# Optimization experiments

Hardware: AMD Instinct MI355X
Metric: run time of the kernel (lower is better)

The kernel has to match this reference:

```python
import jax, jax.numpy as jnp
from jax import lax
import numpy as np

NODE = 5
LAST_F = 64  # hidden_size // node_num = 320 // 5
EPS = 1e-5


def setup_inputs() -> dict:
    key = jax.random.key(0)
    ks = jax.random.split(key, 16)
    B, T = 8192, 512
    x = jax.random.normal(ks[0], (B, NODE, 1, T), dtype=jnp.float32)
    adj = jax.random.bernoulli(ks[1], 0.5, (NODE, NODE)).astype(jnp.float32)
    g = 0.02  # xavier gain in reset_parameters
    W0 = jax.random.normal(ks[2], (65, 128), jnp.float32) * g
    b0 = jnp.zeros((128,), jnp.float32)
    W1 = jax.random.normal(ks[3], (128, 128), jnp.float32) * g
    b1 = jnp.zeros((128,), jnp.float32)
    W2 = jax.random.normal(ks[4], (128, LAST_F), jnp.float32) * g
    b2 = jnp.zeros((LAST_F,), jnp.float32)
    fc1_w = jax.random.normal(ks[5], (NODE + NODE * LAST_F, 256), jnp.float32) * 0.05
    fc1_b = jnp.zeros((256,), jnp.float32)
    bn_gamma = jnp.ones((256,), jnp.float32)
    bn_beta = jnp.zeros((256,), jnp.float32)
    fc2_w = jax.random.normal(ks[6], (256, 7), jnp.float32) * 0.05
    fc2_b = jnp.zeros((7,), jnp.float32)
    return dict(x=x, adj=adj, W0=W0, b0=b0, W1=W1, b1=b1, W2=W2, b2=b2,
                fc1_w=fc1_w, fc1_b=fc1_b, bn_gamma=bn_gamma, bn_beta=bn_beta,
                fc2_w=fc2_w, fc2_b=fc2_b)


def reference(x, adj, W0, b0, W1, b1, W2, b2, fc1_w, fc1_b, bn_gamma, bn_beta, fc2_w, fc2_b):
    B = x.shape[0]
    T = x.shape[3]
    # [B, node, 1, T] -> [T, B, node]
    xt = jnp.transpose(x.reshape(B, NODE, T), (2, 0, 1))
    A = adj.T  # module stores adj.t()

    def gcn(h, W, b):
        # support = h @ W ; out = A @ support + b   (batched)
        return jnp.einsum('ij,bjf->bif', A, h @ W) + b

    def step(state, x_t):
        h = jnp.concatenate([x_t[:, :, None], state], axis=2)  # [B, node, 1+LAST_F]
        h = jax.nn.relu(gcn(h, W0, b0))
        h = jax.nn.relu(gcn(h, W1, b1))
        h = jnp.tanh(gcn(h, W2, b2))
        return h, None

    state0 = jnp.zeros((B, NODE, LAST_F), x.dtype)
    state, _ = lax.scan(step, state0, xt)

    x_end = xt[-1]  # [B, node]
    xs = jnp.concatenate([x_end, state.reshape(B, -1)], axis=1)  # [B, node+hidden]
    h = jax.nn.relu(xs @ fc1_w + fc1_b)
    # BatchNorm1d in training mode: batch statistics (biased variance)
    mean = jnp.mean(h, axis=0)
    var = jnp.var(h, axis=0)
    h = (h - mean) * jax.lax.rsqrt(var + EPS) * bn_gamma + bn_beta
    logits = h @ fc2_w + fc2_b
    return jax.nn.softmax(logits, axis=1)
```

## Files before the change

kernel.cpp:

```cpp
#include <hip/hip_runtime.h>
#include <math.h>

#define NODE 5
#define TT 512
#define NBATCH 8192
#define NB 16
#define MR (NB*NODE)
#define TB 32
#define XS_DIM 325
#define H2 256
#define EPS 1e-5f

typedef _Float16 h16;
typedef __attribute__((ext_vector_type(8))) _Float16 half8;
typedef __attribute__((ext_vector_type(4))) _Float16 h16x4;
typedef __attribute__((ext_vector_type(2))) _Float16 half2v;
typedef __attribute__((ext_vector_type(4))) float float4v;

__device__ __forceinline__ float rfl_f(float v) {
    return __uint_as_float(__builtin_amdgcn_readfirstlane(__float_as_uint(v)));
}
__device__ __forceinline__ half2v pkrtz(float a, float b) {
    return __builtin_bit_cast(half2v, __builtin_amdgcn_cvt_pkrtz(a, b));
}
__device__ __forceinline__ half2v pkmax0(half2v v) {
    half2v z; z[0] = (h16)0.f; z[1] = (h16)0.f;
    return __builtin_elementwise_max(v, z);
}

__global__ __launch_bounds__(256, 2) void rnn_kernel(
    const float* __restrict__ x, const float* __restrict__ adj,
    const float* __restrict__ W0, const float* __restrict__ b0,
    const float* __restrict__ W1, const float* __restrict__ b1,
    const float* __restrict__ W2, const float* __restrict__ b2,
    float* __restrict__ xs)
{
    __shared__ __align__(16) h16 sGD[2][MR*128];
    __shared__ __align__(16) h16 sGS[MR*64];
    __shared__ h16  sx[2][TB][NODE][16];
    __shared__ float sxg[TB][MR];

    const int tid  = threadIdx.x;
    const int lane = tid & 63;
    const int w    = tid >> 6;
    const int ln   = lane & 15;
    const int q    = lane >> 4;
    const int k0q  = q*8;
    const int bbase = blockIdx.x * NB;

    char* const gd0 = (char*)&sGD[0][0];
    char* const gsB = (char*)&sGS[0];
    const int xorv = (ln & 7) << 3;
    const int rB0 = ln*256 + 2*(( 0 + k0q) ^ xorv);
    const int rB1 = ln*256 + 2*((32 + k0q) ^ xorv);
    const int gR0 = ln*128 + 2*(( 0 + k0q) ^ xorv);
    const int gR1 = ln*128 + 2*((32 + k0q) ^ xorv);
    const int wB0 = ln*256 + 2*(((2*w+0)*16 + q*4) ^ xorv);
    const int wB1 = ln*256 + 2*(((2*w+1)*16 + q*4) ^ xorv);
    const int gW  = ln*128 + 2*((w*16 + q*4) ^ xorv);

    float  af[NODE][NODE];
    half2v ahp[NODE][NODE];
    #pragma unroll
    for (int i = 0; i < NODE; ++i)
        #pragma unroll
        for (int j = 0; j < NODE; ++j) {
            float v = rfl_f(adj[j*NODE + i]);
            af[i][j] = v;
            h16 hv = (h16)v;
            half2v t; t[0] = hv; t[1] = hv;
            ahp[i][j] = t;
        }

    half8 wf0[2][2], wf1f[2][4], wf3[4];
    {
        #pragma unroll
        for (int t2 = 0; t2 < 2; ++t2) {
            int n1 = (2*w+t2)*16 + ln;
            #pragma unroll
            for (int ks = 0; ks < 2; ++ks) {
                half8 f;
                #pragma unroll
                for (int j = 0; j < 8; ++j)
                    f[j] = (h16)W0[(size_t)(1 + ks*32 + k0q + j)*128 + n1];
                wf0[t2][ks] = f;
            }
            #pragma unroll
            for (int ks = 0; ks < 4; ++ks) {
                half8 f;
                #pragma unroll
                for (int j = 0; j < 8; ++j)
                    f[j] = (h16)W1[(size_t)(ks*32 + k0q + j)*128 + n1];
                wf1f[t2][ks] = f;
            }
        }
        int n3 = w*16 + ln;
        #pragma unroll
        for (int ks = 0; ks < 4; ++ks) {
            half8 f;
            #pragma unroll
            for (int j = 0; j < 8; ++j)
                f[j] = (h16)W2[(size_t)(ks*32 + k0q + j)*64 + n3];
            wf3[ks] = f;
        }
    }
    float4v b0q[2], b1q[2], b2q;
    float w0s[2][4];
    #pragma unroll
    for (int t2 = 0; t2 < 2; ++t2)
        #pragma unroll
        for (int r = 0; r < 4; ++r) {
            int fi = (2*w+t2)*16 + q*4 + r;
            b0q[t2][r] = b0[fi];
            w0s[t2][r] = W0[fi];
            b1q[t2][r] = b1[fi];
        }
    #pragma unroll
    for (int r = 0; r < 4; ++r) b2q[r] = b2[w*16 + q*4 + r];

    for (int i = tid; i < TB*NODE*16; i += 256) {
        int tl = i & 31; int ne = i >> 5; int n = ne >> 4; int e = ne & 15;
        sx[0][tl][n][e] = (h16)x[((size_t)(bbase+e)*NODE + n)*TT + tl];
    }
    for (int i = tid; i < MR*64; i += 256) sGS[i] = (h16)0.f;
    __syncthreads();

    #pragma unroll 1
    for (int tc = 0; tc < TT/TB; ++tc) {
        const int buf = tc & 1;
        for (int i = tid; i < TB*MR; i += 256) {
            int ti = i / MR, row = i - ti*MR;
            int nd = row >> 4, e = row & 15;
            float acc = 0.f;
            #pragma unroll
            for (int j = 0; j < NODE; ++j)
                acc += af[nd][j] * (float)sx[buf][ti][j][e];
            sxg[ti][row] = acc;
        }
        if (tc+1 < TT/TB) {
            for (int i = tid; i < TB*NODE*16; i += 256) {
                int tl = i & 31; int ne = i >> 5; int n = ne >> 4; int e = ne & 15;
                sx[buf^1][tl][n][e] =
                    (h16)x[((size_t)(bbase+e)*NODE + n)*TT + (tc+1)*TB + tl];
            }
        }
        __syncthreads();

        #pragma unroll 1
        for (int tt = 0; tt < TB; ++tt) {
            const int t = tc*TB + tt;
            const float* sxp = &sxg[tt][ln];
            {
                half2v g[2][NODE][2];
                #pragma unroll
                for (int nd = 0; nd < NODE; ++nd) {
                    half8 a0 = *(const half8*)(gsB + gR0 + nd*2048);
                    half8 a1 = *(const half8*)(gsB + gR1 + nd*2048);
                    float xg = sxp[nd*16];
                    #pragma unroll
                    for (int t2 = 0; t2 < 2; ++t2) {
                        float4v acc = __builtin_amdgcn_mfma_f32_16x16x32_f16(wf0[t2][0], a0, b0q[t2], 0,0,0);
                        acc = __builtin_amdgcn_mfma_f32_16x16x32_f16(wf0[t2][1], a1, acc, 0,0,0);
                        float v0 = fmaf(xg, w0s[t2][0], acc[0]);
                        float v1 = fmaf(xg, w0s[t2][1], acc[1]);
                        float v2 = fmaf(xg, w0s[t2][2], acc[2]);
                        float v3 = fmaf(xg, w0s[t2][3], acc[3]);
                        half2v p0 = pkmax0(pkrtz(v0, v1));
                        half2v p1 = pkmax0(pkrtz(v2, v3));
                        if (nd == 0) {
                            #pragma unroll
                            for (int i = 0; i < NODE; ++i) {
                                g[t2][i][0] = ahp[i][0]*p0;
                                g[t2][i][1] = ahp[i][0]*p1;
                            }
                        } else {
                            #pragma unroll
                            for (int i = 0; i < NODE; ++i) {
                                g[t2][i][0] += ahp[i][nd]*p0;
                                g[t2][i][1] += ahp[i][nd]*p1;
                            }
                        }
                    }
                }
                #pragma unroll
                for (int t2 = 0; t2 < 2; ++t2)
                    #pragma unroll
                    for (int i = 0; i < NODE; ++i) {
                        h16x4 o;
                        o[0]=g[t2][i][0][0]; o[1]=g[t2][i][0][1];
                        o[2]=g[t2][i][1][0]; o[3]=g[t2][i][1][1];
                        *(h16x4*)(gd0 + (t2 ? wB1 : wB0) + i*4096) = o;
                    }
            }
            __syncthreads();
            {
                half2v g[2][NODE][2];
                #pragma unroll
                for (int nd = 0; nd < NODE; ++nd) {
                    half8 a[4];
                    a[0] = *(const half8*)(gd0 + rB0 +       nd*4096);
                    a[1] = *(const half8*)(gd0 + rB1 +       nd*4096);
                    a[2] = *(const half8*)(gd0 + rB0 + 128 + nd*4096);
                    a[3] = *(const half8*)(gd0 + rB1 + 128 + nd*4096);
                    #pragma unroll
                    for (int t2 = 0; t2 < 2; ++t2) {
                        float4v acc = __builtin_amdgcn_mfma_f32_16x16x32_f16(wf1f[t2][0], a[0], b1q[t2], 0,0,0);
                        #pragma unroll
                        for (int ks = 1; ks < 4; ++ks)
                            acc = __builtin_amdgcn_mfma_f32_16x16x32_f16(wf1f[t2][ks], a[ks], acc, 0,0,0);
                        half2v p0 = pkmax0(pkrtz(acc[0], acc[1]));
                        half2v p1 = pkmax0(pkrtz(acc[2], acc[3]));
                        if (nd == 0) {
                            #pragma unroll
                            for (int i = 0; i < NODE; ++i) {
                                g[t2][i][0] = ahp[i][0]*p0;
                                g[t2][i][1] = ahp[i][0]*p1;
                            }
                        } else {
                            #pragma unroll
                            for (int i = 0; i < NODE; ++i) {
                                g[t2][i][0] += ahp[i][nd]*p0;
                                g[t2][i][1] += ahp[i][nd]*p1;
                            }
                        }
                    }
                }
                #pragma unroll
                for (int t2 = 0; t2 < 2; ++t2)
                    #pragma unroll
                    for (int i = 0; i < NODE; ++i) {
                        h16x4 o;
                        o[0]=g[t2][i][0][0]; o[1]=g[t2][i][0][1];
                        o[2]=g[t2][i][1][0]; o[3]=g[t2][i][1][1];
                        *(h16x4*)(gd0 + 20480 + (t2 ? wB1 : wB0) + i*4096) = o;
                    }
            }
            __syncthreads();
            {
                const bool last = (t == TT-1);
                float gs[NODE][4];
                #pragma unroll
                for (int nd = 0; nd < NODE; ++nd) {
                    half8 a[4];
                    a[0] = *(const half8*)(gd0 + 20480 + rB0 +       nd*4096);
                    a[1] = *(const half8*)(gd0 + 20480 + rB1 +       nd*4096);
                    a[2] = *(const half8*)(gd0 + 20480 + rB0 + 128 + nd*4096);
                    a[3] = *(const half8*)(gd0 + 20480 + rB1 + 128 + nd*4096);
                    float4v acc = __builtin_amdgcn_mfma_f32_16x16x32_f16(wf3[0], a[0], b2q, 0,0,0);
                    #pragma unroll
                    for (int ks = 1; ks < 4; ++ks)
                        acc = __builtin_amdgcn_mfma_f32_16x16x32_f16(wf3[ks], a[ks], acc, 0,0,0);
                    float th[4];
                    #pragma unroll
                    for (int r = 0; r < 4; ++r) {
                        float z = acc[r];
                        float e = __expf(-2.f*fabsf(z));
                        float rc = __builtin_amdgcn_rcpf(1.f + e);
                        th[r] = copysignf((1.f - e)*rc, z);
                    }
                    if (last) {
                        size_t ob = (size_t)(bbase+ln)*XS_DIM + 5 + nd*64 + w*16 + q*4;
                        #pragma unroll
                        for (int r = 0; r < 4; ++r) xs[ob + r] = th[r];
                    }
                    if (nd == 0) {
                        #pragma unroll
                        for (int r = 0; r < 4; ++r)
                            #pragma unroll
                            for (int i = 0; i < NODE; ++i) gs[i][r] = af[i][0]*th[r];
                    } else {
                        #pragma unroll
                        for (int r = 0; r < 4; ++r)
                            #pragma unroll
                            for (int i = 0; i < NODE; ++i) gs[i][r] += af[i][nd]*th[r];
                    }
                }
                #pragma unroll
                for (int i = 0; i < NODE; ++i) {
                    h16x4 o;
                    #pragma unroll
                    for (int r = 0; r < 4; ++r) o[r] = (h16)gs[i][r];
                    *(h16x4*)(gsB + gW + i*2048) = o;
                }
            }
            __syncthreads();
        }
    }

    if (tid < NB*NODE) {
        int e = tid / NODE, j = tid - (tid/NODE)*NODE;
        xs[(size_t)(bbase+e)*XS_DIM + j] = (float)sx[1][TB-1][j][e];
    }
}

__global__ __launch_bounds__(256) void fc1_kernel(
    const float* __restrict__ xs, const float* __restrict__ fc1_w,
    const float* __restrict__ fc1_b, float* __restrict__ h,
    float* __restrict__ sums)
{
    __shared__ float s_xs[16*XS_DIM];
    const int tid = threadIdx.x;
    const int r0 = blockIdx.x * 16;
    for (int i = tid; i < 16*XS_DIM; i += 256)
        s_xs[i] = xs[(size_t)r0*XS_DIM + i];
    __syncthreads();

    float acc[16];
    #pragma unroll
    for (int r = 0; r < 16; ++r) acc[r] = 0.f;
    for (int k = 0; k < XS_DIM; ++k) {
        float wv = fc1_w[(size_t)k*H2 + tid];
        #pragma unroll
        for (int r = 0; r < 16; ++r) acc[r] += s_xs[r*XS_DIM + k]*wv;
    }
    float bb = fc1_b[tid];
    float ls = 0.f, lq = 0.f;
    #pragma unroll
    for (int r = 0; r < 16; ++r) {
        float v = fmaxf(acc[r] + bb, 0.f);
        h[(size_t)(r0+r)*H2 + tid] = v;
        ls += v; lq += v*v;
    }
    atomicAdd(&sums[tid], ls);
    atomicAdd(&sums[H2 + tid], lq);
}

__global__ __launch_bounds__(256) void head_kernel(
    const float* __restrict__ h, const float* __restrict__ sums,
    const float* __restrict__ gamma, const float* __restrict__ beta,
    const float* __restrict__ fc2_w, const float* __restrict__ fc2_b,
    float* __restrict__ out)
{
    const int lane = threadIdx.x & 63;
    const int r = blockIdx.x*4 + (threadIdx.x >> 6);
    const int c0 = lane*4;

    float4 hv = *(const float4*)&h[(size_t)r*H2 + c0];
    float hvv[4] = {hv.x, hv.y, hv.z, hv.w};
    float y[4];
    #pragma unroll
    for (int c = 0; c < 4; ++c) {
        int cc = c0 + c;
        float mean = sums[cc] * (1.f/NBATCH);
        float var  = sums[H2+cc]*(1.f/NBATCH) - mean*mean;
        float rstd = rsqrtf(var + EPS);
        y[c] = (hvv[c] - mean)*rstd*gamma[cc] + beta[cc];
    }
    float lg[7];
    #pragma unroll
    for (int j = 0; j < 7; ++j) {
        float p = 0.f;
        #pragma unroll
        for (int c = 0; c < 4; ++c) p += y[c]*fc2_w[(size_t)(c0+c)*7 + j];
        #pragma unroll
        for (int off = 32; off >= 1; off >>= 1) p += __shfl_xor(p, off, 64);
        lg[j] = p + fc2_b[j];
    }
    if (lane == 0) {
        float m = lg[0];
        #pragma unroll
        for (int j = 1; j < 7; ++j) m = fmaxf(m, lg[j]);
        float ev[7]; float s = 0.f;
        #pragma unroll
        for (int j = 0; j < 7; ++j) { ev[j] = expf(lg[j]-m); s += ev[j]; }
        float inv = 1.f/s;
        #pragma unroll
        for (int j = 0; j < 7; ++j) out[(size_t)r*7 + j] = ev[j]*inv;
    }
}

extern "C" void kernel_launch(void* const* d_in, const int* in_sizes, int n_in,
                              void* d_out, int out_size, void* d_ws, size_t ws_size,
                              hipStream_t stream)
{
    (void)in_sizes; (void)n_in; (void)out_size; (void)ws_size;
    const float* x     = (const float*)d_in[0];
    const float* adj   = (const float*)d_in[1];
    const float* W0    = (const float*)d_in[2];
    const float* b0    = (const float*)d_in[3];
    const float* W1    = (const float*)d_in[4];
    const float* b1    = (const float*)d_in[5];
    const float* W2    = (const float*)d_in[6];
    const float* b2    = (const float*)d_in[7];
    const float* fc1w  = (const float*)d_in[8];
    const float* fc1b  = (const float*)d_in[9];
    const float* gamma = (const float*)d_in[10];
    const float* beta  = (const float*)d_in[11];
    const float* fc2w  = (const float*)d_in[12];
    const float* fc2b  = (const float*)d_in[13];
    float* out = (float*)d_out;

    char* ws = (char*)d_ws;
    float* xs   = (float*)(ws);
    float* hbuf = (float*)(ws + 10649600);
    float* sums = (float*)(ws + 10649600 + 8388608);

    hipMemsetAsync(sums, 0, 512*sizeof(float), stream);
    rnn_kernel<<<NBATCH/NB, 256, 0, stream>>>(x, adj, W0, b0, W1, b1, W2, b2, xs);
    fc1_kernel<<<NBATCH/16, 256, 0, stream>>>(xs, fc1w, fc1b, hbuf, sums);
    head_kernel<<<NBATCH/4, 256, 0, stream>>>(hbuf, sums, gamma, beta, fc2w, fc2b, out);
}
```

Measured before the change: 2.316 ms.

## Fold x input into MFMA, add setprio around MFMA loops, cheaper tanh

The scalar x*W0[0] contribution moves into an extra MFMA with a zero-padded half8 operand, which removes the per-element fmaf work and stores the aggregated x in fp16 shared memory. MFMA sections are wrapped in s_setprio(1)/(0) to favour waves that are issuing matrix instructions. Tanh is rewritten as a clamp plus exp2 and rcp, dropping the abs/copysign ops. This adds one MFMA per node and tile and lowers x precision to fp16.

```diff
diff --git a/kernel.cpp b/kernel.cpp
--- a/kernel.cpp
+++ b/kernel.cpp
@@ -38,7 +38,7 @@
     __shared__ __align__(16) h16 sGD[2][MR*128];
     __shared__ __align__(16) h16 sGS[MR*64];
     __shared__ h16  sx[2][TB][NODE][16];
-    __shared__ float sxg[TB][MR];
+    __shared__ h16  sxg[TB][MR];
 
     const int tid  = threadIdx.x;
     const int lane = tid & 63;
@@ -72,7 +72,7 @@
             ahp[i][j] = t;
         }
 
-    half8 wf0[2][2], wf1f[2][4], wf3[4];
+    half8 wf0[2][2], wf0x[2], wf1f[2][4], wf3[4];
     {
         #pragma unroll
         for (int t2 = 0; t2 < 2; ++t2) {
@@ -84,6 +84,13 @@
                 for (int j = 0; j < 8; ++j)
                     f[j] = (h16)W0[(size_t)(1 + ks*32 + k0q + j)*128 + n1];
                 wf0[t2][ks] = f;
+            }
+            {
+                half8 f;
+                #pragma unroll
+                for (int j = 0; j < 8; ++j) f[j] = (h16)0.f;
+                if (q == 0) f[0] = (h16)W0[n1];
+                wf0x[t2] = f;
             }
             #pragma unroll
             for (int ks = 0; ks < 4; ++ks) {
@@ -105,14 +112,12 @@
         }
     }
     float4v b0q[2], b1q[2], b2q;
-    float w0s[2][4];
     #pragma unroll
     for (int t2 = 0; t2 < 2; ++t2)
         #pragma unroll
         for (int r = 0; r < 4; ++r) {
             int fi = (2*w+t2)*16 + q*4 + r;
             b0q[t2][r] = b0[fi];
-            w0s[t2][r] = W0[fi];
             b1q[t2][r] = b1[fi];
         }
     #pragma unroll
@@ -135,7 +140,7 @@
             #pragma unroll
             for (int j = 0; j < NODE; ++j)
                 acc += af[nd][j] * (float)sx[buf][ti][j][e];
-            sxg[ti][row] = acc;
+            sxg[ti][row] = (h16)acc;
         }
         if (tc+1 < TT/TB) {
             for (int i = tid; i < TB*NODE*16; i += 256) {
@@ -149,24 +154,25 @@
         #pragma unroll 1
         for (int tt = 0; tt < TB; ++tt) {
             const int t = tc*TB + tt;
-            const float* sxp = &sxg[tt][ln];
             {
                 half2v g[2][NODE][2];
+                __builtin_amdgcn_s_setprio(1);
                 #pragma unroll
                 for (int nd = 0; nd < NODE; ++nd) {
                     half8 a0 = *(const half8*)(gsB + gR0 + nd*2048);
                     half8 a1 = *(const half8*)(gsB + gR1 + nd*2048);
-                    float xg = sxp[nd*16];
+                    h16 xgv = sxg[tt][nd*16 + ln];
+                    half8 a2;
+                    #pragma unroll
+                    for (int j = 0; j < 8; ++j) a2[j] = (h16)0.f;
+                    if (q == 0) a2[0] = xgv;
                     #pragma unroll
                     for (int t2 = 0; t2 < 2; ++t2) {
-                        float4v acc = __builtin_amdgcn_mfma_f32_16x16x32_f16(wf0[t2][0], a0, b0q[t2], 0,0,0);
+                        float4v acc = __builtin_amdgcn_mfma_f32_16x16x32_f16(wf0x[t2], a2, b0q[t2], 0,0,0);
+                        acc = __builtin_amdgcn_mfma_f32_16x16x32_f16(wf0[t2][0], a0, acc, 0,0,0);
                         acc = __builtin_amdgcn_mfma_f32_16x16x32_f16(wf0[t2][1], a1, acc, 0,0,0);
-                        float v0 = fmaf(xg, w0s[t2][0], acc[0]);
-                        float v1 = fmaf(xg, w0s[t2][1], acc[1]);
-                        float v2 = fmaf(xg, w0s[t2][2], acc[2]);
-                        float v3 = fmaf(xg, w0s[t2][3], acc[3]);
-                        half2v p0 = pkmax0(pkrtz(v0, v1));
-                        half2v p1 = pkmax0(pkrtz(v2, v3));
+                        half2v p0 = pkmax0(pkrtz(acc[0], acc[1]));
+                        half2v p1 = pkmax0(pkrtz(acc[2], acc[3]));
                         if (nd == 0) {
                             #pragma unroll
                             for (int i = 0; i < NODE; ++i) {
@@ -182,6 +188,7 @@
                         }
                     }
                 }
+                __builtin_amdgcn_s_setprio(0);
                 #pragma unroll
                 for (int t2 = 0; t2 < 2; ++t2)
                     #pragma unroll
@@ -195,6 +202,7 @@
             __syncthreads();
             {
                 half2v g[2][NODE][2];
+                __builtin_amdgcn_s_setprio(1);
                 #pragma unroll
                 for (int nd = 0; nd < NODE; ++nd) {
                     half8 a[4];
@@ -225,6 +233,7 @@
                         }
                     }
                 }
+                __builtin_amdgcn_s_setprio(0);
                 #pragma unroll
                 for (int t2 = 0; t2 < 2; ++t2)
                     #pragma unroll
@@ -253,10 +262,9 @@
                     float th[4];
                     #pragma unroll
                     for (int r = 0; r < 4; ++r) {
-                        float z = acc[r];
-                        float e = __expf(-2.f*fabsf(z));
-                        float rc = __builtin_amdgcn_rcpf(1.f + e);
-                        th[r] = copysignf((1.f - e)*rc, z);
+                        float zc = __builtin_amdgcn_fmed3f(acc[r], -9.f, 9.f);
+                        float E  = __builtin_amdgcn_exp2f(zc * 2.885390082f);
+                        th[r] = (E - 1.f) * __builtin_amdgcn_rcpf(E + 1.f);
                     }
                     if (last) {
                         size_t ob = (size_t)(bbase+ln)*XS_DIM + 5 + nd*64 + w*16 + q*4;
```

After: 2.193 ms. 5.3% less time.
